# Kernel optimization log

Measured on AMD Instinct MI355X. Metric: run time of the kernel, lower is better.

## Reference

```python
import jax, jax.numpy as jnp
import numpy as np

N_USERS, N_ITEMS, NNZ, D = 200000, 100000, 5000000, 128


def setup_inputs() -> dict:
    key = jax.random.key(0)
    k1, k2, k3, k4 = jax.random.split(key, 4)
    rows = jax.random.randint(k1, (NNZ,), 0, N_USERS)
    cols = jax.random.randint(k2, (NNZ,), 0, N_ITEMS)
    vals = jax.random.uniform(k3, (NNZ,), dtype=jnp.float32)
    x = jax.random.normal(k4, (N_ITEMS, D), dtype=jnp.float32)
    return {"vals": vals, "x": x, "rows": rows, "cols": cols,
            "n_users": N_USERS, "n_items": N_ITEMS}


def reference(vals, x, rows, cols, n_users, n_items):
    seg = jax.ops.segment_sum
    # --- get_norm_inter_torch: symmetric degree normalization of bipartite A ---
    user_deg = seg(vals, rows, num_segments=n_users)          # [n_users]
    item_deg = seg(vals, cols, num_segments=n_items)          # [n_items]
    # clamp(min=1) guarantees finiteness, so the isinf fixup in torch is a no-op
    u_dinv = jnp.clip(user_deg, 1.0, None) ** -0.5
    i_dinv = jnp.clip(item_deg, 1.0, None) ** -0.5
    norm_vals = vals * u_dinv[rows] * i_dinv[cols]            # [nnz]
    # --- __mul__: y = A x ; out = x - 2 * (A^T y) ---
    y = seg(norm_vals[:, None] * x[cols], rows, num_segments=n_users)   # [n_users, D]
    z = seg(norm_vals[:, None] * y[rows], cols, num_segments=n_items)   # [n_items, D]
    return x - 2.0 * z
```

## Files before the change

### kernel.cpp

```cpp
#include <hip/hip_runtime.h>
#include <hip/hip_bf16.h>


#define D 128
#define NUSERS 200000
#define RBITS 8
#define CBITS 7
#define NB 782
#define CAPB 7168
#define P1T 1024
#define P1E 20
#define P1EDGES (P1T * P1E)
#define MAXDEG_U 96
#define MAXDEG_I 160

typedef unsigned int uint;
typedef unsigned char uchar;

typedef uint  uint4n  __attribute__((ext_vector_type(4)));
typedef float float4n __attribute__((ext_vector_type(4)));

__device__ __forceinline__ float bflo(uint u) { return __uint_as_float(u << 16); }
__device__ __forceinline__ float bfhi(uint u) { return __uint_as_float(u & 0xFFFF0000u); }
__device__ __forceinline__ uint pack2bf(float a, float b) {
    __hip_bfloat162 t;
    t.x = __float2bfloat16(a);
    t.y = __float2bfloat16(b);
    return *(uint*)&t;
}

__device__ __forceinline__ uint ntload_u32(const uint* p) {
    return __builtin_nontemporal_load(p);
}
__device__ __forceinline__ int ntload_i32(const int* p) {
    return __builtin_nontemporal_load(p);
}
__device__ __forceinline__ uchar ntload_u8(const uchar* p) {
    return __builtin_nontemporal_load(p);
}
__device__ __forceinline__ float4 ntload_f4(const float4* p) {
    float4n v = __builtin_nontemporal_load((const float4n*)p);
    float4 r; r.x = v.x; r.y = v.y; r.z = v.z; r.w = v.w; return r;
}
__device__ __forceinline__ void ntstore_f4(float4* p, const float4& s) {
    float4n v; v.x = s.x; v.y = s.y; v.z = s.z; v.w = s.w;
    __builtin_nontemporal_store(v, (float4n*)p);
}

__global__ void __launch_bounds__(P1T) phase1(const int* __restrict__ rows,
                                              const int* __restrict__ cols,
                                              const float* __restrict__ vals,
                                              uint* __restrict__ binUw0,
                                              uchar* __restrict__ binUrl,
                                              uint* __restrict__ binIw0,
                                              uchar* __restrict__ binIrl,
                                              int* __restrict__ binCurU,
                                              int* __restrict__ binCurI,
                                              int nnz) {
    __shared__ uint sw0[P1EDGES];
    __shared__ unsigned short sbin[P1EDGES];
    __shared__ uchar srl[P1EDGES];
    __shared__ int hist[P1T];
    __shared__ int scanA[P1T];
    __shared__ int adj[P1T];

    int tid = threadIdx.x;
    int bb = blockIdx.x * P1EDGES;
    int n = min(nnz - bb, P1EDGES);

    hist[tid] = 0;
    __syncthreads();
#pragma unroll
    for (int j = 0; j < P1E; ++j) {
        int e = bb + j * P1T + tid;
        if (e < nnz) atomicAdd(&hist[rows[e] >> RBITS], 1);
    }
    __syncthreads();
    {
        int h = hist[tid];
        int gb = 0;
        if (tid < NB && h) gb = atomicAdd(&binCurU[tid], h);
        scanA[tid] = h;
        __syncthreads();
        for (int off = 1; off < P1T; off <<= 1) {
            int v = (tid >= off) ? scanA[tid - off] : 0;
            __syncthreads();
            scanA[tid] += v;
            __syncthreads();
        }
        int myexcl = scanA[tid] - h;
        hist[tid] = myexcl;
        adj[tid] = gb - myexcl;
        __syncthreads();
    }
#pragma unroll
    for (int j = 0; j < P1E; ++j) {
        int e = bb + j * P1T + tid;
        if (e < nnz) {
            int r = rows[e], c = cols[e];
            float v = vals[e];
            uint q15 = (uint)(v * 32767.0f + 0.5f);
            int b = r >> RBITS;
            int p = atomicAdd(&hist[b], 1);
            sw0[p] = ((uint)c << 15) | q15;
            sbin[p] = (unsigned short)b;
            srl[p] = (uchar)(r & ((1 << RBITS) - 1));
        }
    }
    __syncthreads();
    for (int i = tid; i < n; i += P1T) {
        int b = sbin[i];
        int pos = adj[b] + i;
        if (pos < CAPB) {
            size_t o = (size_t)b * CAPB + pos;
            binUw0[o] = sw0[i];
            binUrl[o] = srl[i];
        }
    }
    __syncthreads();

    hist[tid] = 0;
    __syncthreads();
#pragma unroll
    for (int j = 0; j < P1E; ++j) {
        int e = bb + j * P1T + tid;
        if (e < nnz) atomicAdd(&hist[cols[e] >> CBITS], 1);
    }
    __syncthreads();
    {
        int h = hist[tid];
        int gb = 0;
        if (tid < NB && h) gb = atomicAdd(&binCurI[tid], h);
        scanA[tid] = h;
        __syncthreads();
        for (int off = 1; off < P1T; off <<= 1) {
            int v = (tid >= off) ? scanA[tid - off] : 0;
            __syncthreads();
            scanA[tid] += v;
            __syncthreads();
        }
        int myexcl = scanA[tid] - h;
        hist[tid] = myexcl;
        adj[tid] = gb - myexcl;
        __syncthreads();
    }
#pragma unroll
    for (int j = 0; j < P1E; ++j) {
        int e = bb + j * P1T + tid;
        if (e < nnz) {
            int r = rows[e], c = cols[e];
            float v = vals[e];
            uint q14 = (uint)(v * 16383.0f + 0.5f);
            int b = c >> CBITS;
            int p = atomicAdd(&hist[b], 1);
            sw0[p] = ((uint)r << 14) | q14;
            sbin[p] = (unsigned short)b;
            srl[p] = (uchar)(c & ((1 << CBITS) - 1));
        }
    }
    __syncthreads();
    for (int i = tid; i < n; i += P1T) {
        int b = sbin[i];
        int pos = adj[b] + i;
        if (pos < CAPB) {
            size_t o = (size_t)b * CAPB + pos;
            binIw0[o] = sw0[i];
            binIrl[o] = srl[i];
        }
    }
}

__global__ void __launch_bounds__(256) phase2_user(uint* __restrict__ binUw0,
                                                   const uchar* __restrict__ binUrl,
                                                   const int* __restrict__ binCurU,
                                                   int* __restrict__ rstart,
                                                   int* __restrict__ rcnt,
                                                   float* __restrict__ urs,
                                                   int n_users) {
    __shared__ uint sw0[CAPB];
    __shared__ uchar srl[CAPB];
    __shared__ int cnt[256], sdeg[256], start[256];
    int b = blockIdx.x, tid = threadIdx.x;
    long long base = (long long)b * CAPB;
    int n = min(binCurU[b], CAPB);
    cnt[tid] = 0;
    sdeg[tid] = 0;
    __syncthreads();
    for (int i = tid; i < n; i += 256) {
        uint w0 = ntload_u32(&binUw0[base + i]);
        uchar rl = ntload_u8(&binUrl[base + i]);
        sw0[i] = w0;
        srl[i] = rl;
        atomicAdd(&cnt[rl], 1);
        atomicAdd(&sdeg[rl], (int)(w0 & 0x7FFFu));
    }
    __syncthreads();
    start[tid] = cnt[tid];
    __syncthreads();
    for (int off = 1; off < 256; off <<= 1) {
        int v = (tid >= off) ? start[tid - off] : 0;
        __syncthreads();
        start[tid] += v;
        __syncthreads();
    }
    int excl = start[tid] - cnt[tid];
    int r = (b << RBITS) + tid;
    if (r < n_users) {
        rstart[r] = (int)(base + excl);
        rcnt[r] = cnt[tid];
        urs[r] = rsqrtf(fmaxf((float)sdeg[tid] * (1.0f / 32767.0f), 1.0f));
    }
    __syncthreads();
    start[tid] = excl;
    __syncthreads();
    for (int i = tid; i < n; i += 256) {
        int rl = srl[i];
        int p = atomicAdd(&start[rl], 1);
        binUw0[base + p] = sw0[i];
    }
}

__global__ void __launch_bounds__(256) phase2_item(uint* __restrict__ binIw0,
                                                   const uchar* __restrict__ binIrl,
                                                   const int* __restrict__ binCurI,
                                                   int* __restrict__ cstart,
                                                   int* __restrict__ ccnt,
                                                   float* __restrict__ irs,
                                                   int n_items) {
    __shared__ uint sw0[CAPB];
    __shared__ uchar srl[CAPB];
    __shared__ int cnt[256], sdeg[256], start[256];
    int b = blockIdx.x, tid = threadIdx.x;
    long long base = (long long)b * CAPB;
    int n = min(binCurI[b], CAPB);
    cnt[tid] = 0;
    sdeg[tid] = 0;
    __syncthreads();
    for (int i = tid; i < n; i += 256) {
        uint w0 = ntload_u32(&binIw0[base + i]);
        uchar cl = ntload_u8(&binIrl[base + i]);
        sw0[i] = w0;
        srl[i] = cl;
        atomicAdd(&cnt[cl], 1);
        atomicAdd(&sdeg[cl], (int)(w0 & 0x3FFFu));
    }
    __syncthreads();
    start[tid] = cnt[tid];
    __syncthreads();
    for (int off = 1; off < 256; off <<= 1) {
        int v = (tid >= off) ? start[tid - off] : 0;
        __syncthreads();
        start[tid] += v;
        __syncthreads();
    }
    int excl = start[tid] - cnt[tid];
    if (tid < (1 << CBITS)) {
        int c = (b << CBITS) + tid;
        if (c < n_items) {
            cstart[c] = (int)(base + excl);
            ccnt[c] = cnt[tid];
            irs[c] = rsqrtf(fmaxf((float)sdeg[tid] * (1.0f / 16383.0f), 1.0f));
        }
    }
    __syncthreads();
    start[tid] = excl;
    __syncthreads();
    for (int i = tid; i < n; i += 256) {
        int cl = srl[i];
        int p = atomicAdd(&start[cl], 1);
        binIw0[base + p] = sw0[i];
    }
}

__global__ void xconv(const float4* __restrict__ x4, uint2* __restrict__ xbf, int n) {
    int i = blockIdx.x * blockDim.x + threadIdx.x;
    if (i < n) {
        float4 v = ntload_f4(&x4[i]);
        uint2 o;
        o.x = pack2bf(v.x, v.y);
        o.y = pack2bf(v.z, v.w);
        xbf[i] = o;
    }
}

__device__ __forceinline__ void fma8(float* a, float w, const uint4& v) {
    a[0] += w * bflo(v.x);
    a[1] += w * bfhi(v.x);
    a[2] += w * bflo(v.y);
    a[3] += w * bfhi(v.y);
    a[4] += w * bflo(v.z);
    a[5] += w * bfhi(v.z);
    a[6] += w * bflo(v.w);
    a[7] += w * bfhi(v.w);
}

__global__ void __launch_bounds__(64) gather_y(const uint* __restrict__ csrU,
                                               const int* __restrict__ rstart,
                                               const int* __restrict__ rcnt,
                                               const float* __restrict__ irs,
                                               const float* __restrict__ urs,
                                               const uint4* __restrict__ xbf4,
                                               uint4* __restrict__ ybf4) {
    __shared__ int sc[MAXDEG_U];
    __shared__ float sw[MAXDEG_U];
    int row = blockIdx.x;
    int lane = threadIdx.x;
    int m = min(rcnt[row], MAXDEG_U);
    int beg = rstart[row];
    for (int i = lane; i < m; i += 64) {
        uint p = ntload_u32(&csrU[beg + i]);
        int c = (int)(p >> 15);
        sc[i] = c;
        sw[i] = (float)(p & 0x7FFFu) * (1.0f / 32767.0f) * irs[c];
    }
    __syncthreads();
    int q = lane >> 4, l = lane & 15;
    float a[8] = {0, 0, 0, 0, 0, 0, 0, 0};
    int k = q;
    for (; k + 12 < m; k += 16) {
        float w0 = sw[k];      uint4 v0 = xbf4[(long long)sc[k] * 16 + l];
        float w1 = sw[k + 4];  uint4 v1 = xbf4[(long long)sc[k + 4] * 16 + l];
        float w2 = sw[k + 8];  uint4 v2 = xbf4[(long long)sc[k + 8] * 16 + l];
        float w3 = sw[k + 12]; uint4 v3 = xbf4[(long long)sc[k + 12] * 16 + l];
        fma8(a, w0, v0);
        fma8(a, w1, v1);
        fma8(a, w2, v2);
        fma8(a, w3, v3);
    }
    for (; k + 4 < m; k += 8) {
        float w0 = sw[k];     uint4 v0 = xbf4[(long long)sc[k] * 16 + l];
        float w1 = sw[k + 4]; uint4 v1 = xbf4[(long long)sc[k + 4] * 16 + l];
        fma8(a, w0, v0);
        fma8(a, w1, v1);
    }
    for (; k < m; k += 4) {
        float w = sw[k];
        uint4 v = xbf4[(long long)sc[k] * 16 + l];
        fma8(a, w, v);
    }
#pragma unroll
    for (int i = 0; i < 8; ++i) {
        a[i] += __shfl_xor(a[i], 16, 64);
        a[i] += __shfl_xor(a[i], 32, 64);
    }
    if (lane < 16) {
        float u = urs[row];
        uint4 o;
        o.x = pack2bf(u * a[0], u * a[1]);
        o.y = pack2bf(u * a[2], u * a[3]);
        o.z = pack2bf(u * a[4], u * a[5]);
        o.w = pack2bf(u * a[6], u * a[7]);
        ybf4[(long long)row * 16 + lane] = o;
    }
}

__global__ void __launch_bounds__(64) gather_z(const uint* __restrict__ csrI,
                                               const int* __restrict__ cstart,
                                               const int* __restrict__ ccnt,
                                               const float* __restrict__ urs,
                                               const float* __restrict__ irs,
                                               const uint4* __restrict__ ybf4,
                                               const float4* __restrict__ x4,
                                               float4* __restrict__ out4) {
    __shared__ int sr[MAXDEG_I];
    __shared__ float sw[MAXDEG_I];
    int col = blockIdx.x;
    int lane = threadIdx.x;
    int m = min(ccnt[col], MAXDEG_I);
    int beg = cstart[col];
    for (int i = lane; i < m; i += 64) {
        uint p = ntload_u32(&csrI[beg + i]);
        int r = (int)(p >> 14);
        sr[i] = r;
        sw[i] = (float)(p & 0x3FFFu) * (1.0f / 16383.0f) * urs[r];
    }
    __syncthreads();
    int q = lane >> 4, l = lane & 15;
    float a[8] = {0, 0, 0, 0, 0, 0, 0, 0};
    int k = q;
    for (; k + 12 < m; k += 16) {
        float w0 = sw[k];      uint4 v0 = ybf4[(long long)sr[k] * 16 + l];
        float w1 = sw[k + 4];  uint4 v1 = ybf4[(long long)sr[k + 4] * 16 + l];
        float w2 = sw[k + 8];  uint4 v2 = ybf4[(long long)sr[k + 8] * 16 + l];
        float w3 = sw[k + 12]; uint4 v3 = ybf4[(long long)sr[k + 12] * 16 + l];
        fma8(a, w0, v0);
        fma8(a, w1, v1);
        fma8(a, w2, v2);
        fma8(a, w3, v3);
    }
    for (; k + 4 < m; k += 8) {
        float w0 = sw[k];     uint4 v0 = ybf4[(long long)sr[k] * 16 + l];
        float w1 = sw[k + 4]; uint4 v1 = ybf4[(long long)sr[k + 4] * 16 + l];
        fma8(a, w0, v0);
        fma8(a, w1, v1);
    }
    for (; k < m; k += 4) {
        float w = sw[k];
        uint4 v = ybf4[(long long)sr[k] * 16 + l];
        fma8(a, w, v);
    }
#pragma unroll
    for (int i = 0; i < 8; ++i) {
        a[i] += __shfl_xor(a[i], 16, 64);
        a[i] += __shfl_xor(a[i], 32, 64);
    }
    if (lane < 16) {
        float ic2 = 2.0f * irs[col];
        long long ob = (long long)col * 32 + l * 2;
        float4 xv0 = ntload_f4(&x4[ob]);
        float4 xv1 = ntload_f4(&x4[ob + 1]);
        float4 o0, o1;
        o0.x = xv0.x - ic2 * a[0];
        o0.y = xv0.y - ic2 * a[1];
        o0.z = xv0.z - ic2 * a[2];
        o0.w = xv0.w - ic2 * a[3];
        o1.x = xv1.x - ic2 * a[4];
        o1.y = xv1.y - ic2 * a[5];
        o1.z = xv1.z - ic2 * a[6];
        o1.w = xv1.w - ic2 * a[7];
        ntstore_f4(&out4[ob], o0);
        ntstore_f4(&out4[ob + 1], o1);
    }
}

extern "C" void kernel_launch(void* const* d_in, const int* in_sizes, int n_in,
                              void* d_out, int out_size, void* d_ws, size_t ws_size,
                              hipStream_t stream) {
    const float* vals = (const float*)d_in[0];
    const float* x    = (const float*)d_in[1];
    const int*   rows = (const int*)d_in[2];
    const int*   cols = (const int*)d_in[3];
    const int nnz     = in_sizes[0];
    const int n_items = in_sizes[1] / D;
    const int n_users = NUSERS;
    float* out = (float*)d_out;

    char* w = (char*)d_ws;
    uint*  binUw0 = (uint*)w;  w += (size_t)NB * CAPB * 4;
    uint*  binIw0 = (uint*)w;  w += (size_t)NB * CAPB * 4;
    uint4* ybf    = (uint4*)w; w += (size_t)n_users * 16 * 16;
    uint4* xbf    = (uint4*)w; w += (size_t)n_items * 16 * 16;
    uchar* binUrl = (uchar*)w; w += (size_t)NB * CAPB;
    uchar* binIrl = (uchar*)w; w += (size_t)NB * CAPB;
    int* rstart = (int*)w;  w += (size_t)n_users * 4;
    int* rcnt   = (int*)w;  w += (size_t)n_users * 4;
    float* urs  = (float*)w; w += (size_t)n_users * 4;
    int* cstart = (int*)w;  w += (size_t)n_items * 4;
    int* ccnt   = (int*)w;  w += (size_t)n_items * 4;
    float* irs  = (float*)w; w += (size_t)n_items * 4;
    char* z0 = w;
    int* binCurU = (int*)w; w += (size_t)NB * 4;
    int* binCurI = (int*)w; w += (size_t)NB * 4;
    size_t zbytes = (size_t)(w - z0);

    hipMemsetAsync(z0, 0, zbytes, stream);

    {
        int n = n_items * 32;
        xconv<<<(n + 255) / 256, 256, 0, stream>>>((const float4*)x, (uint2*)xbf, n);
    }
    {
        int blocks = (nnz + P1EDGES - 1) / P1EDGES;
        phase1<<<blocks, P1T, 0, stream>>>(rows, cols, vals, binUw0, binUrl,
                                           binIw0, binIrl, binCurU, binCurI, nnz);
    }
    phase2_user<<<NB, 256, 0, stream>>>(binUw0, binUrl, binCurU, rstart, rcnt, urs, n_users);
    phase2_item<<<NB, 256, 0, stream>>>(binIw0, binIrl, binCurI, cstart, ccnt, irs, n_items);
    gather_y<<<n_users, 64, 0, stream>>>(binUw0, rstart, rcnt, irs, urs, xbf, ybf);
    gather_z<<<n_items, 64, 0, stream>>>(binIw0, cstart, ccnt, urs, irs, ybf,
                                         (const float4*)x, (float4*)out);
}
```

Measured before the change: 615.3 us.

## Merge user/item histograms in phase1, shrink per-block edges, fuse phase2 kernels

Phase1 now builds the user and item bin histograms in a single pass over rows/cols, removing the second histogram pass and one of its barriers. Edges per block drop from 20 to 8 per thread, which cuts shared memory use and launches more blocks, so occupancy and parallelism rise. The two phase2 kernels are merged into one launch of 2*NB blocks that picks the user or item side from the block index. This removes one launch and lets both sides' bin sorts run concurrently. The cost is more global atomics on binCur and more block-level scans in total, and edges within a bin can land in a different order.

```diff
diff --git a/kernel.cpp b/kernel.cpp
--- a/kernel.cpp
+++ b/kernel.cpp
@@ -9,13 +9,14 @@
 #define NB 782
 #define CAPB 7168
 #define P1T 1024
-#define P1E 20
+#define P1E 8
 #define P1EDGES (P1T * P1E)
 #define MAXDEG_U 96
 #define MAXDEG_I 160
 
 typedef unsigned int uint;
 typedef unsigned char uchar;
+typedef unsigned short ushort;
 
 typedef uint  uint4n  __attribute__((ext_vector_type(4)));
 typedef float float4n __attribute__((ext_vector_type(4)));
@@ -30,9 +31,6 @@
 }
 
 __device__ __forceinline__ uint ntload_u32(const uint* p) {
-    return __builtin_nontemporal_load(p);
-}
-__device__ __forceinline__ int ntload_i32(const int* p) {
     return __builtin_nontemporal_load(p);
 }
 __device__ __forceinline__ uchar ntload_u8(const uchar* p) {
@@ -58,41 +56,67 @@
                                               int* __restrict__ binCurI,
                                               int nnz) {
     __shared__ uint sw0[P1EDGES];
-    __shared__ unsigned short sbin[P1EDGES];
+    __shared__ ushort sbin[P1EDGES];
     __shared__ uchar srl[P1EDGES];
-    __shared__ int hist[P1T];
+    __shared__ int histU[P1T];
+    __shared__ int histI[P1T];
     __shared__ int scanA[P1T];
-    __shared__ int adj[P1T];
+    __shared__ int adjU[P1T];
+    __shared__ int adjI[P1T];
 
     int tid = threadIdx.x;
     int bb = blockIdx.x * P1EDGES;
     int n = min(nnz - bb, P1EDGES);
 
-    hist[tid] = 0;
+    histU[tid] = 0;
+    histI[tid] = 0;
     __syncthreads();
 #pragma unroll
     for (int j = 0; j < P1E; ++j) {
         int e = bb + j * P1T + tid;
-        if (e < nnz) atomicAdd(&hist[rows[e] >> RBITS], 1);
-    }
-    __syncthreads();
+        if (e < nnz) {
+            int r = rows[e], c = cols[e];
+            atomicAdd(&histU[r >> RBITS], 1);
+            atomicAdd(&histI[c >> CBITS], 1);
+        }
+    }
+    __syncthreads();
+
+    int hU = histU[tid];
+    int hI = histI[tid];
+    int gbU = 0, gbI = 0;
+    if (tid < NB && hU) gbU = atomicAdd(&binCurU[tid], hU);
+    if (tid < NB && hI) gbI = atomicAdd(&binCurI[tid], hI);
+
+    scanA[tid] = hU;
+    __syncthreads();
+    for (int off = 1; off < P1T; off <<= 1) {
+        int v = (tid >= off) ? scanA[tid - off] : 0;
+        __syncthreads();
+        scanA[tid] += v;
+        __syncthreads();
+    }
     {
-        int h = hist[tid];
-        int gb = 0;
-        if (tid < NB && h) gb = atomicAdd(&binCurU[tid], h);
-        scanA[tid] = h;
-        __syncthreads();
-        for (int off = 1; off < P1T; off <<= 1) {
-            int v = (tid >= off) ? scanA[tid - off] : 0;
-            __syncthreads();
-            scanA[tid] += v;
-            __syncthreads();
-        }
-        int myexcl = scanA[tid] - h;
-        hist[tid] = myexcl;
-        adj[tid] = gb - myexcl;
-        __syncthreads();
-    }
+        int exU = scanA[tid] - hU;
+        histU[tid] = exU;
+        adjU[tid] = gbU - exU;
+    }
+    __syncthreads();
+    scanA[tid] = hI;
+    __syncthreads();
+    for (int off = 1; off < P1T; off <<= 1) {
+        int v = (tid >= off) ? scanA[tid - off] : 0;
+        __syncthreads();
+        scanA[tid] += v;
+        __syncthreads();
+    }
+    {
+        int exI = scanA[tid] - hI;
+        histI[tid] = exI;
+        adjI[tid] = gbI - exI;
+    }
+    __syncthreads();
+
 #pragma unroll
     for (int j = 0; j < P1E; ++j) {
         int e = bb + j * P1T + tid;
@@ -101,16 +125,16 @@
             float v = vals[e];
             uint q15 = (uint)(v * 32767.0f + 0.5f);
             int b = r >> RBITS;
-            int p = atomicAdd(&hist[b], 1);
+            int p = atomicAdd(&histU[b], 1);
             sw0[p] = ((uint)c << 15) | q15;
-            sbin[p] = (unsigned short)b;
+            sbin[p] = (ushort)b;
             srl[p] = (uchar)(r & ((1 << RBITS) - 1));
         }
     }
     __syncthreads();
     for (int i = tid; i < n; i += P1T) {
         int b = sbin[i];
-        int pos = adj[b] + i;
+        int pos = adjU[b] + i;
         if (pos < CAPB) {
             size_t o = (size_t)b * CAPB + pos;
             binUw0[o] = sw0[i];
@@ -119,31 +143,6 @@
     }
     __syncthreads();
 
-    hist[tid] = 0;
-    __syncthreads();
-#pragma unroll
-    for (int j = 0; j < P1E; ++j) {
-        int e = bb + j * P1T + tid;
-        if (e < nnz) atomicAdd(&hist[cols[e] >> CBITS], 1);
-    }
-    __syncthreads();
-    {
-        int h = hist[tid];
-        int gb = 0;
-        if (tid < NB && h) gb = atomicAdd(&binCurI[tid], h);
-        scanA[tid] = h;
-        __syncthreads();
-        for (int off = 1; off < P1T; off <<= 1) {
-            int v = (tid >= off) ? scanA[tid - off] : 0;
-            __syncthreads();
-            scanA[tid] += v;
-            __syncthreads();
-        }
-        int myexcl = scanA[tid] - h;
-        hist[tid] = myexcl;
-        adj[tid] = gb - myexcl;
-        __syncthreads();
-    }
 #pragma unroll
     for (int j = 0; j < P1E; ++j) {
         int e = bb + j * P1T + tid;
@@ -152,16 +151,16 @@
             float v = vals[e];
             uint q14 = (uint)(v * 16383.0f + 0.5f);
             int b = c >> CBITS;
-            int p = atomicAdd(&hist[b], 1);
+            int p = atomicAdd(&histI[b], 1);
             sw0[p] = ((uint)r << 14) | q14;
-            sbin[p] = (unsigned short)b;
+            sbin[p] = (ushort)b;
             srl[p] = (uchar)(c & ((1 << CBITS) - 1));
         }
     }
     __syncthreads();
     for (int i = tid; i < n; i += P1T) {
         int b = sbin[i];
-        int pos = adj[b] + i;
+        int pos = adjI[b] + i;
         if (pos < CAPB) {
             size_t o = (size_t)b * CAPB + pos;
             binIw0[o] = sw0[i];
@@ -170,29 +169,41 @@
     }
 }
 
-__global__ void __launch_bounds__(256) phase2_user(uint* __restrict__ binUw0,
-                                                   const uchar* __restrict__ binUrl,
-                                                   const int* __restrict__ binCurU,
-                                                   int* __restrict__ rstart,
-                                                   int* __restrict__ rcnt,
-                                                   float* __restrict__ urs,
-                                                   int n_users) {
+__global__ void __launch_bounds__(256) phase2(uint* __restrict__ binUw0,
+                                              const uchar* __restrict__ binUrl,
+                                              const int* __restrict__ binCurU,
+                                              int* __restrict__ rstart,
+                                              int* __restrict__ rcnt,
+                                              float* __restrict__ urs,
+                                              int n_users,
+                                              uint* __restrict__ binIw0,
+                                              const uchar* __restrict__ binIrl,
+                                              const int* __restrict__ binCurI,
+                                              int* __restrict__ cstart,
+                                              int* __restrict__ ccnt,
+                                              float* __restrict__ irs,
+                                              int n_items) {
     __shared__ uint sw0[CAPB];
     __shared__ uchar srl[CAPB];
     __shared__ int cnt[256], sdeg[256], start[256];
-    int b = blockIdx.x, tid = threadIdx.x;
+    int tid = threadIdx.x;
+    bool userSide = (blockIdx.x < NB);
+    int b = userSide ? blockIdx.x : blockIdx.x - NB;
+    uint* binW0 = userSide ? binUw0 : binIw0;
+    const uchar* binRl = userSide ? binUrl : binIrl;
     long long base = (long long)b * CAPB;
-    int n = min(binCurU[b], CAPB);
+    int n = min(userSide ? binCurU[b] : binCurI[b], CAPB);
+    uint vmask = userSide ? 0x7FFFu : 0x3FFFu;
     cnt[tid] = 0;
     sdeg[tid] = 0;
     __syncthreads();
     for (int i = tid; i < n; i += 256) {
-        uint w0 = ntload_u32(&binUw0[base + i]);
-        uchar rl = ntload_u8(&binUrl[base + i]);
+        uint w0 = ntload_u32(&binW0[base + i]);
+        uchar rl = ntload_u8(&binRl[base + i]);
         sw0[i] = w0;
         srl[i] = rl;
         atomicAdd(&cnt[rl], 1);
-        atomicAdd(&sdeg[rl], (int)(w0 & 0x7FFFu));
+        atomicAdd(&sdeg[rl], (int)(w0 & vmask));
     }
     __syncthreads();
     start[tid] = cnt[tid];
@@ -204,57 +215,14 @@
         __syncthreads();
     }
     int excl = start[tid] - cnt[tid];
-    int r = (b << RBITS) + tid;
-    if (r < n_users) {
-        rstart[r] = (int)(base + excl);
-        rcnt[r] = cnt[tid];
-        urs[r] = rsqrtf(fmaxf((float)sdeg[tid] * (1.0f / 32767.0f), 1.0f));
-    }
-    __syncthreads();
-    start[tid] = excl;
-    __syncthreads();
-    for (int i = tid; i < n; i += 256) {
-        int rl = srl[i];
-        int p = atomicAdd(&start[rl], 1);
-        binUw0[base + p] = sw0[i];
-    }
-}
-
-__global__ void __launch_bounds__(256) phase2_item(uint* __restrict__ binIw0,
-                                                   const uchar* __restrict__ binIrl,
-                                                   const int* __restrict__ binCurI,
-                                                   int* __restrict__ cstart,
-                                                   int* __restrict__ ccnt,
-                                                   float* __restrict__ irs,
-                                                   int n_items) {
-    __shared__ uint sw0[CAPB];
-    __shared__ uchar srl[CAPB];
-    __shared__ int cnt[256], sdeg[256], start[256];
-    int b = blockIdx.x, tid = threadIdx.x;
-    long long base = (long long)b * CAPB;
-    int n = min(binCurI[b], CAPB);
-    cnt[tid] = 0;
-    sdeg[tid] = 0;
-    __syncthreads();
-    for (int i = tid; i < n; i += 256) {
-        uint w0 = ntload_u32(&binIw0[base + i]);
-        uchar cl = ntload_u8(&binIrl[base + i]);
-        sw0[i] = w0;
-        srl[i] = cl;
-        atomicAdd(&cnt[cl], 1);
-        atomicAdd(&sdeg[cl], (int)(w0 & 0x3FFFu));
-    }
-    __syncthreads();
-    start[tid] = cnt[tid];
-    __syncthreads();
-    for (int off = 1; off < 256; off <<= 1) {
-        int v = (tid >= off) ? start[tid - off] : 0;
-        __syncthreads();
-        start[tid] += v;
-        __syncthreads();
-    }
-    int excl = start[tid] - cnt[tid];
-    if (tid < (1 << CBITS)) {
+    if (userSide) {
+        int r = (b << RBITS) + tid;
+        if (r < n_users) {
+            rstart[r] = (int)(base + excl);
+            rcnt[r] = cnt[tid];
+            urs[r] = rsqrtf(fmaxf((float)sdeg[tid] * (1.0f / 32767.0f), 1.0f));
+        }
+    } else if (tid < (1 << CBITS)) {
         int c = (b << CBITS) + tid;
         if (c < n_items) {
             cstart[c] = (int)(base + excl);
@@ -266,9 +234,9 @@
     start[tid] = excl;
     __syncthreads();
     for (int i = tid; i < n; i += 256) {
-        int cl = srl[i];
-        int p = atomicAdd(&start[cl], 1);
-        binIw0[base + p] = sw0[i];
+        int rl = srl[i];
+        int p = atomicAdd(&start[rl], 1);
+        binW0[base + p] = sw0[i];
     }
 }
 
@@ -464,8 +432,8 @@
         phase1<<<blocks, P1T, 0, stream>>>(rows, cols, vals, binUw0, binUrl,
                                            binIw0, binIrl, binCurU, binCurI, nnz);
     }
-    phase2_user<<<NB, 256, 0, stream>>>(binUw0, binUrl, binCurU, rstart, rcnt, urs, n_users);
-    phase2_item<<<NB, 256, 0, stream>>>(binIw0, binIrl, binCurI, cstart, ccnt, irs, n_items);
+    phase2<<<2 * NB, 256, 0, stream>>>(binUw0, binUrl, binCurU, rstart, rcnt, urs, n_users,
+                                       binIw0, binIrl, binCurI, cstart, ccnt, irs, n_items);
     gather_y<<<n_users, 64, 0, stream>>>(binUw0, rstart, rcnt, irs, urs, xbf, ybf);
     gather_z<<<n_items, 64, 0, stream>>>(binIw0, cstart, ccnt, urs, irs, ybf,
                                          (const float4*)x, (float4*)out);
```

After: 625.9 us. Within noise of the previous version (+1.7%).
